# Performance work log

Hardware: AMD Instinct MI355X
Metric: run time of the kernel (lower is better)

The kernel has to match this reference:

```python
import jax, jax.numpy as jnp
import numpy as np

T, B, I, H = 1024, 64, 512, 512


def setup_inputs() -> dict:
    key = jax.random.key(0)
    ks = jax.random.split(key, 16)
    s = 0.05  # weight init scale
    inp = {
        "x": jax.random.normal(ks[0], (T, B, I), jnp.float32),
        "h0": jax.random.normal(ks[1], (B, H), jnp.float32),
        "c0": jax.random.normal(ks[2], (B, H), jnp.float32),
        "W_ih0f": jax.random.normal(ks[3], (4 * H, I), jnp.float32) * s,
        "W_hh0f": jax.random.normal(ks[4], (4 * H, H), jnp.float32) * s,
        "b0f": jax.random.normal(ks[5], (4 * H,), jnp.float32) * s,
        "W_ih0b": jax.random.normal(ks[6], (4 * H, I), jnp.float32) * s,
        "W_hh0b": jax.random.normal(ks[7], (4 * H, H), jnp.float32) * s,
        "b0b": jax.random.normal(ks[8], (4 * H,), jnp.float32) * s,
        "W_ih1f": jax.random.normal(ks[9], (4 * H, 2 * H), jnp.float32) * s,
        "W_hh1f": jax.random.normal(ks[10], (4 * H, H), jnp.float32) * s,
        "b1f": jax.random.normal(ks[11], (4 * H,), jnp.float32) * s,
        "W_ih1b": jax.random.normal(ks[12], (4 * H, 2 * H), jnp.float32) * s,
        "W_hh1b": jax.random.normal(ks[13], (4 * H, H), jnp.float32) * s,
        "b1b": jax.random.normal(ks[14], (4 * H,), jnp.float32) * s,
    }
    return inp


def _lstm_dir(x, h0, c0, W_ih, W_hh, b, reverse):
    # x: [T, B, in]; precompute input contribution once (big GEMM)
    xg = jnp.einsum('tbi,gi->tbg', x, W_ih) + b  # [T, B, 4H]

    def step(carry, xt):
        h, c = carry
        g = xt + h @ W_hh.T  # [B, 4H]
        i, f, gg, o = jnp.split(g, 4, axis=-1)  # PyTorch LSTMCell gate order
        i = jax.nn.sigmoid(i)
        f = jax.nn.sigmoid(f)
        gg = jnp.tanh(gg)
        o = jax.nn.sigmoid(o)
        c2 = f * c + i * gg
        h2 = o * jnp.tanh(c2)
        return (h2, c2), h2

    (hT, cT), out = jax.lax.scan(step, (h0, c0), xg, reverse=reverse)
    return out, hT, cT  # out[t] aligned with input time t


def reference(x, h0, c0,
              W_ih0f, W_hh0f, b0f, W_ih0b, W_hh0b, b0b,
              W_ih1f, W_hh1f, b1f, W_ih1b, W_hh1b, b1b):
    layers = [
        ((W_ih0f, W_hh0f, b0f), (W_ih0b, W_hh0b, b0b)),
        ((W_ih1f, W_hh1f, b1f), (W_ih1b, W_hh1b, b1b)),
    ]
    inputs = x
    hn, cn = [], []
    for (fw, bw) in layers:
        # NOTE: original reuses the same init_hidden for every layer/direction
        out_f, hf, cf = _lstm_dir(inputs, h0, c0, *fw, reverse=False)
        out_b, hb, cb = _lstm_dir(inputs, h0, c0, *bw, reverse=True)
        hn.append(jnp.concatenate([hf, hb], axis=1))
        cn.append(jnp.concatenate([cf, cb], axis=1))
        inputs = jnp.concatenate([out_f, out_b], axis=2)  # [T, B, 2H]
    hn = jnp.stack(hn, axis=0)  # [L, B, 2H]
    cn = jnp.stack(cn, axis=0)
    return inputs, hn, cn
```

## Files before the change

kernel.cpp:

```cpp
#include <hip/hip_runtime.h>


using bfrag = __attribute__((ext_vector_type(8))) short;
using facc  = __attribute__((ext_vector_type(4))) float;

#define TT 1024
#define NB 64

#define FENCE_PRE(v)  asm volatile("s_nop 3" : "+v"(v))
#define FENCE_POST(v) asm volatile("s_nop 7\n\ts_nop 7" : "+v"(v))

__device__ __forceinline__ unsigned short f2bf(float f) {
  union { float f; unsigned u; } v; v.f = f;
  unsigned r = v.u + 0x7fffu + ((v.u >> 16) & 1u);
  return (unsigned short)(r >> 16);
}
__device__ __forceinline__ float sigm(float x)  { return 1.f / (1.f + __expf(-x)); }
__device__ __forceinline__ float tanhf_(float x){ return 1.f - 2.f / (__expf(2.f * x) + 1.f); }

__device__ __forceinline__ facc mfma_bf16(bfrag a, bfrag b, facc c) {
  asm("v_mfma_f32_16x16x32_bf16 %0, %1, %2, %0" : "+v"(c) : "v"(a), "v"(b));
  return c;
}

__global__ __launch_bounds__(256) void k_cvt_x(const float* __restrict__ x,
                                               unsigned short* __restrict__ xb) {
  int i = blockIdx.x * 256 + threadIdx.x;
  float4 v = reinterpret_cast<const float4*>(x)[i];
  ushort4 o;
  o.x = f2bf(v.x); o.y = f2bf(v.y); o.z = f2bf(v.z); o.w = f2bf(v.w);
  reinterpret_cast<ushort4*>(xb)[i] = o;
}

__global__ __launch_bounds__(256) void k_init(const float* __restrict__ h0,
                                              const float* __restrict__ c0,
                                              unsigned short* __restrict__ h0b,
                                              float* __restrict__ C4) {
  int i = blockIdx.x * 256 + threadIdx.x;
  h0b[i] = f2bf(h0[i]);
  float c = c0[i];
  C4[i] = c; C4[32768 + i] = c; C4[65536 + i] = c; C4[98304 + i] = c;
}

template <int KX>
__global__ __launch_bounds__(256) void k_pack(const float* __restrict__ Wih,
                                              const float* __restrict__ Whh,
                                              const float* __restrict__ bias,
                                              unsigned short* __restrict__ PW,
                                              float* __restrict__ PB) {
  constexpr int K = KX + 512;
  int tid = blockIdx.x * 256 + threadIdx.x;
  int R = tid / K;
  int k = tid - R * K;
  int g = R >> 4, r = R & 15;
  int q = r >> 2, gate = r & 3;
  int srow = gate * 512 + (g * 4 + q);
  float v = (k < KX) ? Wih[srow * KX + k] : Whh[srow * 512 + (k - KX)];
  PW[tid] = f2bf(v);
  if (k == 0) PB[R] = bias[srow];
}

template <int LAYER>
__global__ __launch_bounds__(256) void k_step(
    int s,
    const unsigned short* __restrict__ xin,
    unsigned short* __restrict__ y0,
    float* __restrict__ dout,
    const unsigned short* __restrict__ h0b,
    float* __restrict__ C4,
    unsigned short* __restrict__ hb,
    const unsigned short* __restrict__ PWf, const unsigned short* __restrict__ PWb,
    const float* __restrict__ PBf, const float* __restrict__ PBb) {
  constexpr int KX = (LAYER == 0) ? 512 : 1024;
  constexpr int K  = KX + 512;

  const int bid  = blockIdx.x;
  const int dir  = bid >> 7;
  const int hg   = bid & 127;
  const int t    = dir ? (TT - 1 - s) : s;
  const int wave = threadIdx.x >> 6;
  const int lane = threadIdx.x & 63;
  const int lr   = lane & 15;
  const int lq   = lane >> 4;
  const int b    = wave * 16 + lr;
  const bool first = (s == 0);
  const int tprev  = dir ? (t + 1) : (t - 1);

  const unsigned short* pw = dir ? PWb : PWf;
  const float* pb          = dir ? PBb : PBf;
  const unsigned short* Abase = pw + (size_t)(hg * 16 + lr) * K + lq * 8;

  const unsigned short* xrow = xin + ((size_t)t * NB + b) * (size_t)KX + lq * 8;

  const unsigned short* hrow;
  if (first)            hrow = h0b + (size_t)b * 512 + lq * 8;
  else if (LAYER == 0)  hrow = y0 + ((size_t)tprev * NB + b) * 1024 + dir * 512 + lq * 8;
  else                  hrow = hb + (size_t)((((s & 1) ^ 1) * 2 + dir)) * 32768 + (size_t)b * 512 + lq * 8;

  facc acc = {0.f, 0.f, 0.f, 0.f};
  FENCE_PRE(acc);

#pragma unroll 8
  for (int kk = 0; kk < KX / 32; ++kk) {
    bfrag a = *reinterpret_cast<const bfrag*>(Abase + kk * 32);
    bfrag x = *reinterpret_cast<const bfrag*>(xrow + kk * 32);
    acc = mfma_bf16(a, x, acc);
  }
#pragma unroll 8
  for (int kk = 0; kk < 16; ++kk) {
    bfrag a = *reinterpret_cast<const bfrag*>(Abase + KX + kk * 32);
    bfrag h = *reinterpret_cast<const bfrag*>(hrow + kk * 32);
    acc = mfma_bf16(a, h, acc);
  }
  FENCE_POST(acc);

  const int hcol = hg * 4 + lq;
  const int scan = LAYER * 2 + dir;
  float4 bias = *reinterpret_cast<const float4*>(pb + hg * 16 + lq * 4);
  float ig = sigm(acc[0] + bias.x);
  float fg = sigm(acc[1] + bias.y);
  float gv = tanhf_(acc[2] + bias.z);
  float og = sigm(acc[3] + bias.w);
  const int cidx = scan * 32768 + b * 512 + hcol;
  float c2 = fg * C4[cidx] + ig * gv;
  float h2 = og * tanhf_(c2);
  C4[cidx] = c2;

  const size_t orow = ((size_t)t * NB + b) * 1024 + dir * 512 + hcol;
  if (LAYER == 0) {
    y0[orow] = f2bf(h2);
  } else {
    dout[orow] = h2;
    hb[(size_t)((s & 1) * 2 + dir) * 32768 + (size_t)b * 512 + hcol] = f2bf(h2);
  }

  if (s == TT - 1) {
    const size_t oh = ((size_t)LAYER * NB + b) * 1024 + dir * 512 + hcol;
    dout[67108864 + oh] = h2;
    dout[67239936 + oh] = c2;
  }
}

extern "C" void kernel_launch(void* const* d_in, const int* in_sizes, int n_in,
                              void* d_out, int out_size, void* d_ws, size_t ws_size,
                              hipStream_t stream) {
  (void)in_sizes; (void)n_in; (void)out_size; (void)ws_size;
  const float* x  = (const float*)d_in[0];
  const float* h0 = (const float*)d_in[1];
  const float* c0 = (const float*)d_in[2];
  const float* W[12];
  for (int i = 0; i < 12; ++i) W[i] = (const float*)d_in[3 + i];

  char* ws = (char*)d_ws;
  unsigned short* xb   = (unsigned short*)(ws + 0ull);
  unsigned short* y0   = (unsigned short*)(ws + 67108864ull);
  unsigned short* h0b  = (unsigned short*)(ws + 201326592ull);
  unsigned short* PW0F = (unsigned short*)(ws + 201392128ull);
  unsigned short* PW0B = (unsigned short*)(ws + 205586432ull);
  unsigned short* PW1F = (unsigned short*)(ws + 209780736ull);
  unsigned short* PW1B = (unsigned short*)(ws + 216072192ull);
  float*          PB   = (float*)(ws + 222363648ull);
  float*          C4   = (float*)(ws + 222396416ull);
  unsigned short* hb   = (unsigned short*)(ws + 222920704ull);
  float* dout = (float*)d_out;

  k_cvt_x<<<32768, 256, 0, stream>>>(x, xb);
  k_init<<<128, 256, 0, stream>>>(h0, c0, h0b, C4);
  k_pack<512> <<<8192, 256, 0, stream>>>(W[0], W[1],  W[2],  PW0F, PB + 0);
  k_pack<512> <<<8192, 256, 0, stream>>>(W[3], W[4],  W[5],  PW0B, PB + 2048);
  k_pack<1024><<<12288, 256, 0, stream>>>(W[6], W[7],  W[8],  PW1F, PB + 4096);
  k_pack<1024><<<12288, 256, 0, stream>>>(W[9], W[10], W[11], PW1B, PB + 6144);

  for (int s = 0; s < TT; ++s)
    k_step<0><<<256, 256, 0, stream>>>(s, xb, y0, dout, h0b, C4, hb, PW0F, PW0B, PB + 0,    PB + 2048);
  for (int s = 0; s < TT; ++s)
    k_step<1><<<256, 256, 0, stream>>>(s, y0, y0, dout, h0b, C4, hb, PW1F, PW1B, PB + 4096, PB + 6144);
}
```

Baseline: 25.58 ms.

## Replace per-timestep launches with persistent cooperative scan kernel using LDS-resident weights

Replaces the 2048 per-step kernel launches with one persistent cooperative kernel per layer. Each block keeps its slice of packed weights in LDS and the cell state in registers, and the blocks of each direction synchronize through an atomic counter spin-wait. The input-projection MFMAs are issued before the wait so they overlap the barrier latency. This removes launch overhead and repeated global weight reads, but relies on all 128 blocks being co-resident and on correct acquire/release ordering.

```diff
diff --git a/kernel.cpp b/kernel.cpp
--- a/kernel.cpp
+++ b/kernel.cpp
@@ -6,9 +6,6 @@
 
 #define TT 1024
 #define NB 64
-
-#define FENCE_PRE(v)  asm volatile("s_nop 3" : "+v"(v))
-#define FENCE_POST(v) asm volatile("s_nop 7\n\ts_nop 7" : "+v"(v))
 
 __device__ __forceinline__ unsigned short f2bf(float f) {
   union { float f; unsigned u; } v; v.f = f;
@@ -33,13 +30,11 @@
 }
 
 __global__ __launch_bounds__(256) void k_init(const float* __restrict__ h0,
-                                              const float* __restrict__ c0,
                                               unsigned short* __restrict__ h0b,
-                                              float* __restrict__ C4) {
+                                              unsigned* __restrict__ cnts) {
   int i = blockIdx.x * 256 + threadIdx.x;
   h0b[i] = f2bf(h0[i]);
-  float c = c0[i];
-  C4[i] = c; C4[32768 + i] = c; C4[65536 + i] = c; C4[98304 + i] = c;
+  if (i < 4) cnts[i * 1024] = 0;
 }
 
 template <int KX>
@@ -56,88 +51,109 @@
   int q = r >> 2, gate = r & 3;
   int srow = gate * 512 + (g * 4 + q);
   float v = (k < KX) ? Wih[srow * KX + k] : Whh[srow * 512 + (k - KX)];
-  PW[tid] = f2bf(v);
+  int gb = R >> 5, rr = R & 31, cc = k >> 3;
+  PW[(size_t)gb * (K / 8) * 272 + cc * 272 + rr * 8 + (k & 7)] = f2bf(v);
   if (k == 0) PB[R] = bias[srow];
 }
 
 template <int LAYER>
-__global__ __launch_bounds__(256) void k_step(
-    int s,
+__global__ __launch_bounds__(512, 2) void k_scan(
     const unsigned short* __restrict__ xin,
     unsigned short* __restrict__ y0,
     float* __restrict__ dout,
     const unsigned short* __restrict__ h0b,
-    float* __restrict__ C4,
+    const float* __restrict__ c0,
     unsigned short* __restrict__ hb,
     const unsigned short* __restrict__ PWf, const unsigned short* __restrict__ PWb,
-    const float* __restrict__ PBf, const float* __restrict__ PBb) {
+    const float* __restrict__ PBf, const float* __restrict__ PBb,
+    unsigned* __restrict__ cntF, unsigned* __restrict__ cntB) {
   constexpr int KX = (LAYER == 0) ? 512 : 1024;
   constexpr int K  = KX + 512;
-
-  const int bid  = blockIdx.x;
-  const int dir  = bid >> 7;
-  const int hg   = bid & 127;
-  const int t    = dir ? (TT - 1 - s) : s;
-  const int wave = threadIdx.x >> 6;
-  const int lane = threadIdx.x & 63;
-  const int lr   = lane & 15;
-  const int lq   = lane >> 4;
-  const int b    = wave * 16 + lr;
-  const bool first = (s == 0);
-  const int tprev  = dir ? (t + 1) : (t - 1);
-
-  const unsigned short* pw = dir ? PWb : PWf;
+  constexpr int CH = K / 8;
+  extern __shared__ unsigned short Wlds[];
+
+  const int bid = blockIdx.x;
+  const int dir = bid >> 6;
+  const int gb  = bid & 63;
+  const int tid = threadIdx.x;
+  unsigned* cnt = dir ? cntB : cntF;
+  const unsigned short* pw = (dir ? PWb : PWf) + (size_t)gb * CH * 272;
   const float* pb          = dir ? PBb : PBf;
-  const unsigned short* Abase = pw + (size_t)(hg * 16 + lr) * K + lq * 8;
-
-  const unsigned short* xrow = xin + ((size_t)t * NB + b) * (size_t)KX + lq * 8;
-
-  const unsigned short* hrow;
-  if (first)            hrow = h0b + (size_t)b * 512 + lq * 8;
-  else if (LAYER == 0)  hrow = y0 + ((size_t)tprev * NB + b) * 1024 + dir * 512 + lq * 8;
-  else                  hrow = hb + (size_t)((((s & 1) ^ 1) * 2 + dir)) * 32768 + (size_t)b * 512 + lq * 8;
-
-  facc acc = {0.f, 0.f, 0.f, 0.f};
-  FENCE_PRE(acc);
-
+
+  for (int i = tid; i < CH * 34; i += 512)
+    reinterpret_cast<bfrag*>(Wlds)[i] = reinterpret_cast<const bfrag*>(pw)[i];
+  __syncthreads();
+
+  const int w = tid >> 6, lane = tid & 63;
+  const int lr = lane & 15, lq = lane >> 4;
+  const int grT = w & 1, bT = w >> 1;
+  const int b    = bT * 16 + lr;
+  const int hcol = (gb * 2 + grT) * 4 + lq;
+  const int ldsBase = grT * 128 + lr * 8;
+  const float4 bias = *reinterpret_cast<const float4*>(pb + (gb * 2 + grT) * 16 + lq * 4);
+  float c = c0[b * 512 + hcol];
+
+  for (int s = 0; s < TT; ++s) {
+    const int t = dir ? (TT - 1 - s) : s;
+
+    const unsigned short* xrow = xin + ((size_t)t * NB + b) * KX + lq * 8;
+    facc a0 = {0.f, 0.f, 0.f, 0.f}, a1 = {0.f, 0.f, 0.f, 0.f};
+    asm volatile("s_nop 3" : "+v"(a0), "+v"(a1));
 #pragma unroll 8
-  for (int kk = 0; kk < KX / 32; ++kk) {
-    bfrag a = *reinterpret_cast<const bfrag*>(Abase + kk * 32);
-    bfrag x = *reinterpret_cast<const bfrag*>(xrow + kk * 32);
-    acc = mfma_bf16(a, x, acc);
-  }
+    for (int kk = 0; kk < KX / 32; ++kk) {
+      bfrag a = *reinterpret_cast<const bfrag*>(Wlds + (size_t)(kk * 4 + lq) * 272 + ldsBase);
+      bfrag x = *reinterpret_cast<const bfrag*>(xrow + kk * 32);
+      if (kk & 1) a1 = mfma_bf16(a, x, a1); else a0 = mfma_bf16(a, x, a0);
+    }
+
+    if (s > 0) {
+      if (tid == 0) {
+        const unsigned tgt = 64u * (unsigned)s;
+        while (__hip_atomic_load(cnt, __ATOMIC_RELAXED, __HIP_MEMORY_SCOPE_AGENT) < tgt)
+          __builtin_amdgcn_s_sleep(2);
+        __builtin_amdgcn_fence(__ATOMIC_ACQUIRE, "agent");
+      }
+      __syncthreads();
+    }
+
+    const int tp = dir ? (t + 1) : (t - 1);
+    const unsigned short* hrow;
+    if (s == 0)               hrow = h0b + (size_t)b * 512 + lq * 8;
+    else if constexpr (LAYER == 0)
+                              hrow = y0 + ((size_t)tp * NB + b) * 1024 + dir * 512 + lq * 8;
+    else                      hrow = hb + (size_t)(((s & 1) ^ 1) * 2 + dir) * 32768 + (size_t)b * 512 + lq * 8;
 #pragma unroll 8
-  for (int kk = 0; kk < 16; ++kk) {
-    bfrag a = *reinterpret_cast<const bfrag*>(Abase + KX + kk * 32);
-    bfrag h = *reinterpret_cast<const bfrag*>(hrow + kk * 32);
-    acc = mfma_bf16(a, h, acc);
-  }
-  FENCE_POST(acc);
-
-  const int hcol = hg * 4 + lq;
-  const int scan = LAYER * 2 + dir;
-  float4 bias = *reinterpret_cast<const float4*>(pb + hg * 16 + lq * 4);
-  float ig = sigm(acc[0] + bias.x);
-  float fg = sigm(acc[1] + bias.y);
-  float gv = tanhf_(acc[2] + bias.z);
-  float og = sigm(acc[3] + bias.w);
-  const int cidx = scan * 32768 + b * 512 + hcol;
-  float c2 = fg * C4[cidx] + ig * gv;
-  float h2 = og * tanhf_(c2);
-  C4[cidx] = c2;
-
-  const size_t orow = ((size_t)t * NB + b) * 1024 + dir * 512 + hcol;
-  if (LAYER == 0) {
-    y0[orow] = f2bf(h2);
-  } else {
-    dout[orow] = h2;
-    hb[(size_t)((s & 1) * 2 + dir) * 32768 + (size_t)b * 512 + hcol] = f2bf(h2);
-  }
-
-  if (s == TT - 1) {
-    const size_t oh = ((size_t)LAYER * NB + b) * 1024 + dir * 512 + hcol;
-    dout[67108864 + oh] = h2;
-    dout[67239936 + oh] = c2;
+    for (int kk = 0; kk < 16; ++kk) {
+      bfrag a = *reinterpret_cast<const bfrag*>(Wlds + (size_t)(KX / 8 + kk * 4 + lq) * 272 + ldsBase);
+      bfrag h = *reinterpret_cast<const bfrag*>(hrow + kk * 32);
+      if (kk & 1) a1 = mfma_bf16(a, h, a1); else a0 = mfma_bf16(a, h, a0);
+    }
+    asm volatile("s_nop 7\n\ts_nop 7" : "+v"(a0), "+v"(a1));
+
+    float ig = sigm(a0[0] + a1[0] + bias.x);
+    float fg = sigm(a0[1] + a1[1] + bias.y);
+    float gv = tanhf_(a0[2] + a1[2] + bias.z);
+    float og = sigm(a0[3] + a1[3] + bias.w);
+    c = fg * c + ig * gv;
+    const float h2 = og * tanhf_(c);
+
+    const size_t orow = ((size_t)t * NB + b) * 1024 + dir * 512 + hcol;
+    if constexpr (LAYER == 0) {
+      __hip_atomic_store(&y0[orow], f2bf(h2), __ATOMIC_RELAXED, __HIP_MEMORY_SCOPE_AGENT);
+    } else {
+      dout[orow] = h2;
+      __hip_atomic_store(&hb[(size_t)((s & 1) * 2 + dir) * 32768 + (size_t)b * 512 + hcol],
+                         f2bf(h2), __ATOMIC_RELAXED, __HIP_MEMORY_SCOPE_AGENT);
+    }
+    if (s == TT - 1) {
+      const size_t oh = ((size_t)LAYER * NB + b) * 1024 + dir * 512 + hcol;
+      dout[67108864 + oh] = h2;
+      dout[67239936 + oh] = c;
+    }
+
+    __syncthreads();
+    if (tid == 0)
+      __hip_atomic_fetch_add(cnt, 1u, __ATOMIC_RELEASE, __HIP_MEMORY_SCOPE_AGENT);
   }
 }
 
@@ -156,23 +172,44 @@
   unsigned short* y0   = (unsigned short*)(ws + 67108864ull);
   unsigned short* h0b  = (unsigned short*)(ws + 201326592ull);
   unsigned short* PW0F = (unsigned short*)(ws + 201392128ull);
-  unsigned short* PW0B = (unsigned short*)(ws + 205586432ull);
-  unsigned short* PW1F = (unsigned short*)(ws + 209780736ull);
-  unsigned short* PW1B = (unsigned short*)(ws + 216072192ull);
-  float*          PB   = (float*)(ws + 222363648ull);
-  float*          C4   = (float*)(ws + 222396416ull);
-  unsigned short* hb   = (unsigned short*)(ws + 222920704ull);
+  unsigned short* PW0B = (unsigned short*)(ws + 205848576ull);
+  unsigned short* PW1F = (unsigned short*)(ws + 210305024ull);
+  unsigned short* PW1B = (unsigned short*)(ws + 216989696ull);
+  float*          PB   = (float*)(ws + 223674368ull);
+  unsigned short* hb   = (unsigned short*)(ws + 223707136ull);
+  unsigned*       cnts = (unsigned*)(ws + 223969280ull);
   float* dout = (float*)d_out;
 
   k_cvt_x<<<32768, 256, 0, stream>>>(x, xb);
-  k_init<<<128, 256, 0, stream>>>(h0, c0, h0b, C4);
+  k_init<<<128, 256, 0, stream>>>(h0, h0b, cnts);
   k_pack<512> <<<8192, 256, 0, stream>>>(W[0], W[1],  W[2],  PW0F, PB + 0);
   k_pack<512> <<<8192, 256, 0, stream>>>(W[3], W[4],  W[5],  PW0B, PB + 2048);
   k_pack<1024><<<12288, 256, 0, stream>>>(W[6], W[7],  W[8],  PW1F, PB + 4096);
   k_pack<1024><<<12288, 256, 0, stream>>>(W[9], W[10], W[11], PW1B, PB + 6144);
 
-  for (int s = 0; s < TT; ++s)
-    k_step<0><<<256, 256, 0, stream>>>(s, xb, y0, dout, h0b, C4, hb, PW0F, PW0B, PB + 0,    PB + 2048);
-  for (int s = 0; s < TT; ++s)
-    k_step<1><<<256, 256, 0, stream>>>(s, y0, y0, dout, h0b, C4, hb, PW1F, PW1B, PB + 4096, PB + 6144);
-}
+  const unsigned short* xin0 = xb;
+  const unsigned short* xin1 = y0;
+  unsigned short* y0m = y0;
+  unsigned short* y0n = nullptr;
+  const unsigned short* h0bc = h0b;
+  unsigned* c00 = cnts + 0;    unsigned* c01 = cnts + 1024;
+  unsigned* c10 = cnts + 2048; unsigned* c11 = cnts + 3072;
+  const unsigned short *pw0f = PW0F, *pw0b = PW0B, *pw1f = PW1F, *pw1b = PW1B;
+  const float *pb0f = PB + 0, *pb0b = PB + 2048, *pb1f = PB + 4096, *pb1b = PB + 6144;
+
+  void* args0[] = {(void*)&xin0, (void*)&y0m, (void*)&dout, (void*)&h0bc, (void*)&c0,
+                   (void*)&hb, (void*)&pw0f, (void*)&pw0b, (void*)&pb0f, (void*)&pb0b,
+                   (void*)&c00, (void*)&c01};
+  void* args1[] = {(void*)&xin1, (void*)&y0n, (void*)&dout, (void*)&h0bc, (void*)&c0,
+                   (void*)&hb, (void*)&pw1f, (void*)&pw1b, (void*)&pb1f, (void*)&pb1b,
+                   (void*)&c10, (void*)&c11};
+
+  (void)hipFuncSetAttribute((const void*)(&k_scan<0>),
+                            hipFuncAttributeMaxDynamicSharedMemorySize, 69632);
+  (void)hipFuncSetAttribute((const void*)(&k_scan<1>),
+                            hipFuncAttributeMaxDynamicSharedMemorySize, 104448);
+  (void)hipLaunchCooperativeKernel((const void*)(&k_scan<0>), dim3(128), dim3(512),
+                                   args0, 69632, stream);
+  (void)hipLaunchCooperativeKernel((const void*)(&k_scan<1>), dim3(128), dim3(512),
+                                   args1, 104448, stream);
+}
```

Result: faster. 23.47 ms (-8.2%).
